# Kernel optimization log

Hardware: AMD Instinct MI355X
Metric: run time of the kernel (lower is better)

## Reference

```python
import jax, jax.numpy as jnp
import numpy as np

N = 50000   # nodes
E = 600000  # edges
H = 128     # hidden_dim


def _linear_params(key, fan_in, fan_out):
    kw, kb = jax.random.split(key)
    s = 1.0 / np.sqrt(fan_in)
    w = jax.random.uniform(kw, (fan_in, fan_out), minval=-s, maxval=s, dtype=jnp.float32)
    b = jax.random.uniform(kb, (fan_out,), minval=-s, maxval=s, dtype=jnp.float32)
    return w, b


def setup_inputs():
    key = jax.random.key(0)
    ks = jax.random.split(key, 9)
    x = jax.random.uniform(ks[0], (N, 1), dtype=jnp.float32)
    pre_h = jax.random.normal(ks[1], (N, H), dtype=jnp.float32)
    edge_index = jax.random.randint(ks[2], (2, E), 0, N, dtype=jnp.int32)
    edge_attr = jax.random.uniform(ks[3], (E, 1), dtype=jnp.float32)
    enc_w, enc_b = _linear_params(ks[4], 1 + H, H)      # BFS_Encoder.linear
    M_w, M_b = _linear_params(ks[5], H + H + 1, H)      # MPNN_Processor.M
    U_w, U_b = _linear_params(ks[6], H + H, H)          # MPNN_Processor.U
    dec_w, dec_b = _linear_params(ks[7], H + H, 1)      # BFS_Decoder.linear
    ter_w, ter_b = _linear_params(ks[8], H + H, 1)      # BFS_Terminator.linear
    return {"x": x, "pre_h": pre_h, "edge_attr": edge_attr,
            "enc_w": enc_w, "enc_b": enc_b, "M_w": M_w, "M_b": M_b,
            "U_w": U_w, "U_b": U_b, "dec_w": dec_w, "dec_b": dec_b,
            "ter_w": ter_w, "ter_b": ter_b, "edge_index": edge_index}


def reference(x, pre_h, edge_attr, enc_w, enc_b, M_w, M_b, U_w, U_b,
              dec_w, dec_b, ter_w, ter_b, edge_index):
    # Encoder: z = relu(Linear([x, pre_h]))
    z = jax.nn.relu(jnp.concatenate([x, pre_h], axis=-1) @ enc_w + enc_b)  # [N,H]

    # Processor (PyG MessagePassing, flow source_to_target):
    # z_i = z[edge_index[1]] (target), z_j = z[edge_index[0]] (source)
    src, tgt = edge_index[0], edge_index[1]
    m = jax.nn.relu(
        jnp.concatenate([z[tgt], z[src], edge_attr], axis=-1) @ M_w + M_b)  # [E,H]
    # scatter-max aggregate into target nodes; empty segments -> 0
    agg = jax.ops.segment_max(m, tgt, num_segments=N)
    agg = jnp.where(jnp.isfinite(agg), agg, 0.0)
    h = jax.nn.relu(jnp.concatenate([z, agg], axis=-1) @ U_w + U_b)  # [N,H]

    # Decoder
    y = jax.nn.sigmoid(jnp.concatenate([z, h], axis=-1) @ dec_w + dec_b)  # [N,1]

    # Terminator: mean over nodes, broadcast-concat, scalar mean
    h_mean = jnp.broadcast_to(jnp.mean(h, axis=0), h.shape)
    ter = jnp.mean(jnp.concatenate([h, h_mean], axis=-1) @ ter_w + ter_b)
    return h, y, ter
```

## Files before the change

### kernel.cpp

```cpp
#include <hip/hip_runtime.h>
#include <hip/hip_bf16.h>
#include <math.h>

#define HD 128
#define APAD 136

typedef short bf16x8 __attribute__((ext_vector_type(8)));
typedef float f32x4 __attribute__((ext_vector_type(4)));

static __device__ __forceinline__ unsigned short f2bf(float f) {
  __hip_bfloat16 b = __float2bfloat16(f);
  return *(unsigned short*)&b;
}
static __device__ __forceinline__ float bflo(unsigned int u) {
  return __uint_as_float(u << 16);
}
static __device__ __forceinline__ float bfhi(unsigned int u) {
  return __uint_as_float(u & 0xffff0000u);
}

__global__ __launch_bounds__(256) void k_frag_hist(
    const float* __restrict__ enc_w, const float* __restrict__ M_w,
    const float* __restrict__ U_w,
    unsigned short* __restrict__ encf, unsigned short* __restrict__ Pf,
    unsigned short* __restrict__ Qf, unsigned short* __restrict__ Uf,
    const int* __restrict__ ei, int* __restrict__ cnt, int E) {
  const int b = blockIdx.x;
  if (b >= 40) {
    const int e = (b - 40) * 256 + threadIdx.x;
    if (e < E) atomicAdd(&cnt[ei[E + e]], 1);
    return;
  }
  const float* W; unsigned short* F; int KS; int lb;
  if (b < 8)       { W = enc_w + HD;     F = encf; KS = 4; lb = b; }
  else if (b < 16) { W = M_w;            F = Pf;   KS = 4; lb = b - 8; }
  else if (b < 24) { W = M_w + HD * HD;  F = Qf;   KS = 4; lb = b - 16; }
  else             { W = U_w;            F = Uf;   KS = 8; lb = b - 24; }
  const int gid = lb * 256 + threadIdx.x;
  const int lane = gid & 63;
  const int ks = (gid >> 6) % KS;
  const int tile = gid / (64 * KS);
  const int col = tile * 16 + (lane & 15);
  const int k0 = ks * 32 + (lane >> 4) * 8;
  unsigned short v[8];
#pragma unroll
  for (int j = 0; j < 8; ++j) v[j] = f2bf(W[(size_t)(k0 + j) * HD + col]);
  unsigned short* dst = F + ((size_t)(tile * KS + ks) * 64 + lane) * 8;
#pragma unroll
  for (int j = 0; j < 8; ++j) dst[j] = v[j];
}

__global__ __launch_bounds__(256) void k_scan_block(
    const int* __restrict__ cnt, int* __restrict__ row_ptr,
    int* __restrict__ partials, int N) {
  __shared__ int s[256];
  const int t = threadIdx.x;
  const int base = blockIdx.x * 1024 + t * 4;
  int v[4], sum = 0;
#pragma unroll
  for (int i = 0; i < 4; ++i) {
    v[i] = (base + i < N) ? cnt[base + i] : 0;
    sum += v[i];
  }
  s[t] = sum;
  __syncthreads();
  for (int off = 1; off < 256; off <<= 1) {
    int xv = (t >= off) ? s[t - off] : 0;
    __syncthreads();
    if (t >= off) s[t] += xv;
    __syncthreads();
  }
  int run = s[t] - sum;
  if (t == 255) partials[blockIdx.x] = s[255];
#pragma unroll
  for (int i = 0; i < 4; ++i) {
    if (base + i < N) row_ptr[base + i] = run;
    run += v[i];
  }
}

__global__ void k_scan_partials(int* __restrict__ partials, int nb) {
  if (threadIdx.x == 0) {
    int run = 0;
    for (int i = 0; i < nb; ++i) { int v = partials[i]; partials[i] = run; run += v; }
  }
}

__global__ __launch_bounds__(256) void k_scan_add(
    int* __restrict__ row_ptr, const int* __restrict__ partials,
    int* __restrict__ cursor, int N) {
  const int base = blockIdx.x * 1024 + threadIdx.x * 4;
  const int p = partials[blockIdx.x];
#pragma unroll
  for (int i = 0; i < 4; ++i) {
    if (base + i < N) {
      int v = row_ptr[base + i] + p;
      row_ptr[base + i] = v;
      cursor[base + i] = v;
    }
  }
}

__global__ __launch_bounds__(256) void k_scatter(
    const int* __restrict__ ei, const float* __restrict__ edge_attr,
    int* __restrict__ cursor, int2* __restrict__ epack, int E) {
  const int e = blockIdx.x * 256 + threadIdx.x;
  if (e >= E) return;
  const int tgt = ei[E + e];
  const int pos = atomicAdd(&cursor[tgt], 1);
  epack[pos] = make_int2(ei[e], __float_as_int(edge_attr[e]));
}

__global__ __launch_bounds__(256, 4) void k_enc_pq(
    const float* __restrict__ x, const float* __restrict__ pre_h,
    const float* __restrict__ enc_w, const float* __restrict__ enc_b,
    const float* __restrict__ M_b,
    const unsigned short* __restrict__ encf, const unsigned short* __restrict__ Pf,
    const unsigned short* __restrict__ Qf,
    unsigned short* __restrict__ zg, unsigned short* __restrict__ Pg,
    unsigned short* __restrict__ Qg) {
  __shared__ unsigned short phs[16 * APAD];
  __shared__ unsigned short zsh[16 * APAD];
  __shared__ float xs[16];
  const int t = threadIdx.x;
  const int n0 = blockIdx.x * 16;

  {
    const int r = t >> 4, c0 = (t & 15) * 8;
    const float4 a = *(const float4*)&pre_h[(size_t)(n0 + r) * HD + c0];
    const float4 b = *(const float4*)&pre_h[(size_t)(n0 + r) * HD + c0 + 4];
    unsigned short* d = &phs[r * APAD + c0];
    d[0] = f2bf(a.x); d[1] = f2bf(a.y); d[2] = f2bf(a.z); d[3] = f2bf(a.w);
    d[4] = f2bf(b.x); d[5] = f2bf(b.y); d[6] = f2bf(b.z); d[7] = f2bf(b.w);
  }
  if (t < 16) xs[t] = x[n0 + t];
  __syncthreads();

  const int w = t >> 6, l = t & 63;
  const int m = l & 15, q = l >> 4;

  bf16x8 af[4];
#pragma unroll
  for (int ks = 0; ks < 4; ++ks)
    af[ks] = *(const bf16x8*)&phs[m * APAD + ks * 32 + q * 8];
  f32x4 acc[2] = {{0, 0, 0, 0}, {0, 0, 0, 0}};
#pragma unroll
  for (int tt = 0; tt < 2; ++tt) {
    const int tn = 2 * w + tt;
#pragma unroll
    for (int ks = 0; ks < 4; ++ks) {
      const bf16x8 bf = *(const bf16x8*)&encf[((size_t)(tn * 4 + ks) * 64 + l) * 8];
      acc[tt] = __builtin_amdgcn_mfma_f32_16x16x32_bf16(af[ks], bf, acc[tt], 0, 0, 0);
    }
  }
#pragma unroll
  for (int tt = 0; tt < 2; ++tt) {
    const int col = (2 * w + tt) * 16 + m;
    const float bb = enc_b[col];
    const float w0 = enc_w[col];
#pragma unroll
    for (int r = 0; r < 4; ++r) {
      const int row = q * 4 + r;
      const float zv = fmaxf(acc[tt][r] + bb + xs[row] * w0, 0.0f);
      zsh[row * APAD + col] = f2bf(zv);
    }
  }
  __syncthreads();

  bf16x8 az[4];
#pragma unroll
  for (int ks = 0; ks < 4; ++ks)
    az[ks] = *(const bf16x8*)&zsh[m * APAD + ks * 32 + q * 8];
  {
    const int r = t >> 4, c0 = (t & 15) * 8;
    *(uint4*)&zg[(size_t)(n0 + r) * HD + c0] = *(const uint4*)&zsh[r * APAD + c0];
  }
  __syncthreads();

  f32x4 pacc[2] = {{0, 0, 0, 0}, {0, 0, 0, 0}};
  f32x4 qacc[2] = {{0, 0, 0, 0}, {0, 0, 0, 0}};
#pragma unroll
  for (int tt = 0; tt < 2; ++tt) {
    const int tn = 2 * w + tt;
#pragma unroll
    for (int ks = 0; ks < 4; ++ks) {
      const bf16x8 bp = *(const bf16x8*)&Pf[((size_t)(tn * 4 + ks) * 64 + l) * 8];
      const bf16x8 bq = *(const bf16x8*)&Qf[((size_t)(tn * 4 + ks) * 64 + l) * 8];
      pacc[tt] = __builtin_amdgcn_mfma_f32_16x16x32_bf16(az[ks], bp, pacc[tt], 0, 0, 0);
      qacc[tt] = __builtin_amdgcn_mfma_f32_16x16x32_bf16(az[ks], bq, qacc[tt], 0, 0, 0);
    }
  }
#pragma unroll
  for (int tt = 0; tt < 2; ++tt) {
    const int col = (2 * w + tt) * 16 + m;
    const float mb = M_b[col];
#pragma unroll
    for (int r = 0; r < 4; ++r) {
      const int row = q * 4 + r;
      phs[row * APAD + col] = f2bf(pacc[tt][r] + mb);
      zsh[row * APAD + col] = f2bf(qacc[tt][r]);
    }
  }
  __syncthreads();
  {
    const int r = t >> 4, c0 = (t & 15) * 8;
    *(uint4*)&Pg[(size_t)(n0 + r) * HD + c0] = *(const uint4*)&phs[r * APAD + c0];
    *(uint4*)&Qg[(size_t)(n0 + r) * HD + c0] = *(const uint4*)&zsh[r * APAD + c0];
  }
}

__global__ __launch_bounds__(256, 8) void k_gather(
    const unsigned short* __restrict__ Pg, const unsigned short* __restrict__ Qg,
    const float* __restrict__ w_attr,
    const int* __restrict__ row_ptr, const int* __restrict__ row_end,
    const int2* __restrict__ epack,
    unsigned short* __restrict__ ag, int N) {
  const int t = threadIdx.x;
  const int w = t >> 6, l = t & 63;
  const int g = l >> 4, j = l & 15;
  const int n0 = blockIdx.x * 32;

  float wv[8];
  {
    const float4 wa = *(const float4*)&w_attr[j * 8];
    const float4 wb = *(const float4*)&w_attr[j * 8 + 4];
    wv[0] = wa.x; wv[1] = wa.y; wv[2] = wa.z; wv[3] = wa.w;
    wv[4] = wb.x; wv[5] = wb.y; wv[6] = wb.z; wv[7] = wb.w;
  }

#pragma unroll
  for (int i = 0; i < 2; ++i) {
    const int r = w * 8 + g * 2 + i;
    const int n = n0 + r;
    const int nc = min(n, N - 1);
    const int rs = row_ptr[nc], re = row_end[nc];
    float acc[8];
#pragma unroll
    for (int c = 0; c < 8; ++c) acc[c] = -INFINITY;
    for (int e = rs; e < re; e += 4) {
      int2 pk[4];
#pragma unroll
      for (int u = 0; u < 4; ++u) pk[u] = epack[min(e + u, re - 1)];
      uint4 qv[4];
#pragma unroll
      for (int u = 0; u < 4; ++u)
        qv[u] = *(const uint4*)&Qg[(size_t)pk[u].x * HD + j * 8];
#pragma unroll
      for (int u = 0; u < 4; ++u) {
        const float a = __int_as_float(pk[u].y);
        const unsigned int qq[4] = {qv[u].x, qv[u].y, qv[u].z, qv[u].w};
#pragma unroll
        for (int c = 0; c < 4; ++c) {
          acc[2 * c]     = fmaxf(acc[2 * c],     fmaf(a, wv[2 * c],     bflo(qq[c])));
          acc[2 * c + 1] = fmaxf(acc[2 * c + 1], fmaf(a, wv[2 * c + 1], bfhi(qq[c])));
        }
      }
    }
    if (n < N) {
      float res[8];
      if (re > rs) {
        const uint4 pv = *(const uint4*)&Pg[(size_t)n * HD + j * 8];
        const unsigned int pp[4] = {pv.x, pv.y, pv.z, pv.w};
#pragma unroll
        for (int c = 0; c < 4; ++c) {
          res[2 * c]     = fmaxf(bflo(pp[c]) + acc[2 * c],     0.0f);
          res[2 * c + 1] = fmaxf(bfhi(pp[c]) + acc[2 * c + 1], 0.0f);
        }
      } else {
#pragma unroll
        for (int c = 0; c < 8; ++c) res[c] = 0.0f;
      }
      uint4 st;
      st.x = (unsigned)f2bf(res[0]) | ((unsigned)f2bf(res[1]) << 16);
      st.y = (unsigned)f2bf(res[2]) | ((unsigned)f2bf(res[3]) << 16);
      st.z = (unsigned)f2bf(res[4]) | ((unsigned)f2bf(res[5]) << 16);
      st.w = (unsigned)f2bf(res[6]) | ((unsigned)f2bf(res[7]) << 16);
      *(uint4*)&ag[(size_t)n * HD + j * 8] = st;
    }
  }
}

__global__ __launch_bounds__(256, 8) void k_update(
    const unsigned short* __restrict__ zg, const unsigned short* __restrict__ ag,
    const unsigned short* __restrict__ Uf,
    const float* __restrict__ U_b, const float* __restrict__ dec_w,
    const float* __restrict__ dec_b,
    float* __restrict__ h_out, float* __restrict__ y_out,
    float* __restrict__ hpart, int N) {
  __shared__ unsigned short zsh[32 * APAD];
  __shared__ unsigned short ash[32 * APAD];
  __shared__ float hcol[HD];
  __shared__ float dacc[32];
  __shared__ float pr[32][8];
  const int t = threadIdx.x;
  const int n0 = blockIdx.x * 32;

  {
    const int r = t >> 3, c0 = (t & 7) * 16;
    const int n = min(n0 + r, N - 1);
    *(uint4*)&zsh[r * APAD + c0]     = *(const uint4*)&zg[(size_t)n * HD + c0];
    *(uint4*)&zsh[r * APAD + c0 + 8] = *(const uint4*)&zg[(size_t)n * HD + c0 + 8];
    *(uint4*)&ash[r * APAD + c0]     = *(const uint4*)&ag[(size_t)n * HD + c0];
    *(uint4*)&ash[r * APAD + c0 + 8] = *(const uint4*)&ag[(size_t)n * HD + c0 + 8];
  }
  if (t < 32) dacc[t] = 0.0f;
  if (t < HD) hcol[t] = 0.0f;
  __syncthreads();

  const int w = t >> 6, l = t & 63;

  const int mt = w & 1, nh = w >> 1;
  const int m = mt * 16 + (l & 15), q = l >> 4;
  bf16x8 afz[4], afa[4];
#pragma unroll
  for (int ks = 0; ks < 4; ++ks) {
    afz[ks] = *(const bf16x8*)&zsh[m * APAD + ks * 32 + q * 8];
    afa[ks] = *(const bf16x8*)&ash[m * APAD + ks * 32 + q * 8];
  }
  f32x4 acc4[4] = {{0, 0, 0, 0}, {0, 0, 0, 0}, {0, 0, 0, 0}, {0, 0, 0, 0}};
#pragma unroll
  for (int tt = 0; tt < 4; ++tt) {
    const int tn = nh * 4 + tt;
#pragma unroll
    for (int ks = 0; ks < 8; ++ks) {
      const bf16x8 bf = *(const bf16x8*)&Uf[((size_t)(tn * 8 + ks) * 64 + l) * 8];
      const bf16x8 a = (ks < 4) ? afz[ks] : afa[ks - 4];
      acc4[tt] = __builtin_amdgcn_mfma_f32_16x16x32_bf16(a, bf, acc4[tt], 0, 0, 0);
    }
  }
  float dp[4] = {0.0f, 0.0f, 0.0f, 0.0f};
#pragma unroll
  for (int tt = 0; tt < 4; ++tt) {
    const int col = (nh * 4 + tt) * 16 + (l & 15);
    const float ub = U_b[col];
    const float dw = dec_w[HD + col];
    float s4 = 0.0f;
#pragma unroll
    for (int r = 0; r < 4; ++r) {
      const int rowl = mt * 16 + q * 4 + r;
      const int n = n0 + rowl;
      float hv = fmaxf(acc4[tt][r] + ub, 0.0f);
      if (n < N) h_out[(size_t)n * HD + col] = hv; else hv = 0.0f;
      s4 += hv;
      dp[r] += hv * dw;
    }
    atomicAdd(&hcol[col], s4);
  }
#pragma unroll
  for (int off = 1; off < 16; off <<= 1) {
#pragma unroll
    for (int r = 0; r < 4; ++r) dp[r] += __shfl_xor(dp[r], off);
  }
  if ((l & 15) == 0) {
#pragma unroll
    for (int r = 0; r < 4; ++r) atomicAdd(&dacc[mt * 16 + q * 4 + r], dp[r]);
  }

  {
    const int r2 = t >> 3, s = t & 7;
    float part = 0.0f;
#pragma unroll
    for (int c = 0; c < 8; ++c) {
      const int kk = s * 16 + 2 * c;
      const unsigned int zu = *(const unsigned int*)&zsh[r2 * APAD + kk];
      part += bflo(zu) * dec_w[kk] + bfhi(zu) * dec_w[kk + 1];
    }
    pr[r2][s] = part;
  }
  __syncthreads();

  if (t < HD) hpart[(size_t)blockIdx.x * HD + t] = hcol[t];
  if (t < 32 && n0 + t < N) {
    float d = dec_b[0] + dacc[t];
#pragma unroll
    for (int s = 0; s < 8; ++s) d += pr[t][s];
    y_out[n0 + t] = 1.0f / (1.0f + expf(-d));
  }
}

__global__ __launch_bounds__(256) void k_hred(
    const float* __restrict__ hpart, float* __restrict__ hsum, int NB) {
  __shared__ float sh[HD];
  const int t = threadIdx.x;
  const int col = t & (HD - 1);
  const int half = t >> 7;
  float acc = 0.0f;
  for (int r = blockIdx.x * 2 + half; r < NB; r += 32)
    acc += hpart[(size_t)r * HD + col];
  if (half) sh[col] = acc;
  __syncthreads();
  if (!half) atomicAdd(&hsum[col], acc + sh[col]);
}

__global__ __launch_bounds__(128) void k_ter(
    const float* __restrict__ hsum, const float* __restrict__ ter_w,
    const float* __restrict__ ter_b, float* __restrict__ out, float invN) {
  __shared__ float r2[2];
  const int t = threadIdx.x;
  float v = (hsum[t] * invN) * (ter_w[t] + ter_w[HD + t]);
#pragma unroll
  for (int o = 32; o > 0; o >>= 1) v += __shfl_down(v, o);
  if ((t & 63) == 0) r2[t >> 6] = v;
  __syncthreads();
  if (t == 0) out[0] = r2[0] + r2[1] + ter_b[0];
}

extern "C" void kernel_launch(void* const* d_in, const int* in_sizes, int n_in,
                              void* d_out, int out_size, void* d_ws, size_t ws_size,
                              hipStream_t stream) {
  const float* x        = (const float*)d_in[0];
  const float* pre_h    = (const float*)d_in[1];
  const float* edge_attr= (const float*)d_in[2];
  const float* enc_w    = (const float*)d_in[3];
  const float* enc_b    = (const float*)d_in[4];
  const float* M_w      = (const float*)d_in[5];
  const float* M_b      = (const float*)d_in[6];
  const float* U_w      = (const float*)d_in[7];
  const float* U_b      = (const float*)d_in[8];
  const float* dec_w    = (const float*)d_in[9];
  const float* dec_b    = (const float*)d_in[10];
  const float* ter_w    = (const float*)d_in[11];
  const float* ter_b    = (const float*)d_in[12];
  const int*   edge_idx = (const int*)d_in[13];

  const int N = in_sizes[0];
  const int E = in_sizes[2];
  const size_t NH = (size_t)N * HD;

  float* out = (float*)d_out;
  float* h_out = out;
  float* y_out = out + NH;
  float* ter_out = out + NH + N;

  unsigned short* zg = (unsigned short*)d_ws;
  unsigned short* Pg = zg + NH;
  unsigned short* Qg = Pg + NH;
  unsigned short* ag = Qg + NH;
  int*   cursor   = (int*)(ag + NH);
  int*   row_ptr  = cursor + N;
  int*   partials = row_ptr + N;
  float* hsum     = (float*)(partials + 64);
  int2*  epack    = (int2*)(hsum + HD);
  unsigned short* encf = (unsigned short*)(epack + E);
  unsigned short* Pf   = encf + 8 * 4 * 64 * 8;
  unsigned short* Qf   = Pf + 8 * 4 * 64 * 8;
  unsigned short* Uf   = Qf + 8 * 4 * 64 * 8;
  float* hpart = (float*)(Uf + 16 * 256 * 8);

  hipMemsetAsync(cursor, 0, (2 * (size_t)N + 64 + HD) * sizeof(int), stream);

  const int scan_blocks = (N + 1023) / 1024;
  const int eb = (E + 255) / 256;
  const int nb32 = (N + 31) / 32;

  k_frag_hist<<<40 + eb, 256, 0, stream>>>(enc_w, M_w, U_w, encf, Pf, Qf, Uf,
                                           edge_idx, cursor, E);
  k_scan_block<<<scan_blocks, 256, 0, stream>>>(cursor, row_ptr, partials, N);
  k_scan_partials<<<1, 64, 0, stream>>>(partials, scan_blocks);
  k_scan_add<<<scan_blocks, 256, 0, stream>>>(row_ptr, partials, cursor, N);
  k_scatter<<<eb, 256, 0, stream>>>(edge_idx, edge_attr, cursor, epack, E);

  k_enc_pq<<<N / 16, 256, 0, stream>>>(x, pre_h, enc_w, enc_b, M_b,
                                       encf, Pf, Qf, zg, Pg, Qg);
  k_gather<<<nb32, 256, 0, stream>>>(
      Pg, Qg, M_w + 256 * HD, row_ptr, cursor, epack, ag, N);
  k_update<<<nb32, 256, 0, stream>>>(
      zg, ag, Uf, U_b, dec_w, dec_b, h_out, y_out, hpart, N);
  k_hred<<<16, 256, 0, stream>>>(hpart, hsum, nb32);
  k_ter<<<1, 128, 0, stream>>>(hsum, ter_w, ter_b, ter_out, 1.0f / (float)N);
}
```

Baseline: 259.5 us.

## Merge small launches: fold partials scan, fuse scatter with encoder, fuse reduce and terminator

Removes the single-thread partials scan kernel by having each scan_add block reduce the preceding partials itself with a wavefront shuffle. Merges the edge scatter kernel and the encoder/PQ kernel into one launch whose first eb blocks scatter edges while the rest run the encoder, so the two overlap. Replaces the two-kernel h reduction and terminator with a single 1024-thread block, which also drops the hsum buffer and shrinks the memset. The aim is fewer launches and less serialization, at the cost of one block doing all of the hpart reduction and an unused load left in the decoder loop.

```diff
diff --git a/kernel.cpp b/kernel.cpp
--- a/kernel.cpp
+++ b/kernel.cpp
@@ -79,18 +79,20 @@
   }
 }
 
-__global__ void k_scan_partials(int* __restrict__ partials, int nb) {
-  if (threadIdx.x == 0) {
-    int run = 0;
-    for (int i = 0; i < nb; ++i) { int v = partials[i]; partials[i] = run; run += v; }
-  }
-}
-
 __global__ __launch_bounds__(256) void k_scan_add(
     int* __restrict__ row_ptr, const int* __restrict__ partials,
-    int* __restrict__ cursor, int N) {
-  const int base = blockIdx.x * 1024 + threadIdx.x * 4;
-  const int p = partials[blockIdx.x];
+    int* __restrict__ cursor, int N, int nb) {
+  __shared__ int poff;
+  const int t = threadIdx.x;
+  if (t < 64) {
+    int v = (t < nb && t < blockIdx.x) ? partials[t] : 0;
+#pragma unroll
+    for (int o = 32; o > 0; o >>= 1) v += __shfl_down(v, o);
+    if (t == 0) poff = v;
+  }
+  __syncthreads();
+  const int p = poff;
+  const int base = blockIdx.x * 1024 + t * 4;
 #pragma unroll
   for (int i = 0; i < 4; ++i) {
     if (base + i < N) {
@@ -101,17 +103,9 @@
   }
 }
 
-__global__ __launch_bounds__(256) void k_scatter(
+__global__ __launch_bounds__(256, 4) void k_scatter_enc(
     const int* __restrict__ ei, const float* __restrict__ edge_attr,
-    int* __restrict__ cursor, int2* __restrict__ epack, int E) {
-  const int e = blockIdx.x * 256 + threadIdx.x;
-  if (e >= E) return;
-  const int tgt = ei[E + e];
-  const int pos = atomicAdd(&cursor[tgt], 1);
-  epack[pos] = make_int2(ei[e], __float_as_int(edge_attr[e]));
-}
-
-__global__ __launch_bounds__(256, 4) void k_enc_pq(
+    int* __restrict__ cursor, int2* __restrict__ epack, int E, int eb,
     const float* __restrict__ x, const float* __restrict__ pre_h,
     const float* __restrict__ enc_w, const float* __restrict__ enc_b,
     const float* __restrict__ M_b,
@@ -123,8 +117,18 @@
   __shared__ unsigned short zsh[16 * APAD];
   __shared__ float xs[16];
   const int t = threadIdx.x;
-  const int n0 = blockIdx.x * 16;
-
+
+  if (blockIdx.x < (unsigned)eb) {
+    const int e = blockIdx.x * 256 + t;
+    if (e < E) {
+      const int tgt = ei[E + e];
+      const int pos = atomicAdd(&cursor[tgt], 1);
+      epack[pos] = make_int2(ei[e], __float_as_int(edge_attr[e]));
+    }
+    return;
+  }
+
+  const int n0 = (blockIdx.x - eb) * 16;
   {
     const int r = t >> 4, c0 = (t & 15) * 8;
     const float4 a = *(const float4*)&pre_h[(size_t)(n0 + r) * HD + c0];
@@ -363,6 +367,7 @@
     for (int c = 0; c < 8; ++c) {
       const int kk = s * 16 + 2 * c;
       const unsigned int zu = *(const unsigned int*)&zsh[r2 * APAD + kk];
+      const unsigned int hu = *(const unsigned int*)&ash[r2 * APAD + kk];
       part += bflo(zu) * dec_w[kk] + bfhi(zu) * dec_w[kk + 1];
     }
     pr[r2][s] = part;
@@ -378,31 +383,33 @@
   }
 }
 
-__global__ __launch_bounds__(256) void k_hred(
-    const float* __restrict__ hpart, float* __restrict__ hsum, int NB) {
-  __shared__ float sh[HD];
+__global__ __launch_bounds__(1024) void k_hredter(
+    const float* __restrict__ hpart, const float* __restrict__ ter_w,
+    const float* __restrict__ ter_b, float* __restrict__ out,
+    float invN, int NB) {
+  __shared__ float s[1024];
   const int t = threadIdx.x;
   const int col = t & (HD - 1);
-  const int half = t >> 7;
+  const int grp = t >> 7;
   float acc = 0.0f;
-  for (int r = blockIdx.x * 2 + half; r < NB; r += 32)
-    acc += hpart[(size_t)r * HD + col];
-  if (half) sh[col] = acc;
-  __syncthreads();
-  if (!half) atomicAdd(&hsum[col], acc + sh[col]);
-}
-
-__global__ __launch_bounds__(128) void k_ter(
-    const float* __restrict__ hsum, const float* __restrict__ ter_w,
-    const float* __restrict__ ter_b, float* __restrict__ out, float invN) {
-  __shared__ float r2[2];
-  const int t = threadIdx.x;
-  float v = (hsum[t] * invN) * (ter_w[t] + ter_w[HD + t]);
+  for (int r = grp; r < NB; r += 8) acc += hpart[(size_t)r * HD + col];
+  s[t] = acc;
+  __syncthreads();
+  if (t < 512) s[t] += s[t + 512];
+  __syncthreads();
+  if (t < 256) s[t] += s[t + 256];
+  __syncthreads();
+  float v = 0.0f;
+  if (t < 128) {
+    const float colsum = s[t] + s[t + 128];
+    v = (colsum * invN) * (ter_w[t] + ter_w[HD + t]);
+  }
 #pragma unroll
   for (int o = 32; o > 0; o >>= 1) v += __shfl_down(v, o);
-  if ((t & 63) == 0) r2[t >> 6] = v;
-  __syncthreads();
-  if (t == 0) out[0] = r2[0] + r2[1] + ter_b[0];
+  __syncthreads();
+  if (t < 128 && (t & 63) == 0) s[t >> 6] = v;
+  __syncthreads();
+  if (t == 0) out[0] = s[0] + s[1] + ter_b[0];
 }
 
 extern "C" void kernel_launch(void* const* d_in, const int* in_sizes, int n_in,
@@ -439,15 +446,14 @@
   int*   cursor   = (int*)(ag + NH);
   int*   row_ptr  = cursor + N;
   int*   partials = row_ptr + N;
-  float* hsum     = (float*)(partials + 64);
-  int2*  epack    = (int2*)(hsum + HD);
+  int2*  epack    = (int2*)(partials + 64);
   unsigned short* encf = (unsigned short*)(epack + E);
   unsigned short* Pf   = encf + 8 * 4 * 64 * 8;
   unsigned short* Qf   = Pf + 8 * 4 * 64 * 8;
   unsigned short* Uf   = Qf + 8 * 4 * 64 * 8;
   float* hpart = (float*)(Uf + 16 * 256 * 8);
 
-  hipMemsetAsync(cursor, 0, (2 * (size_t)N + 64 + HD) * sizeof(int), stream);
+  hipMemsetAsync(cursor, 0, (size_t)N * sizeof(int), stream);
 
   const int scan_blocks = (N + 1023) / 1024;
   const int eb = (E + 255) / 256;
@@ -456,16 +462,15 @@
   k_frag_hist<<<40 + eb, 256, 0, stream>>>(enc_w, M_w, U_w, encf, Pf, Qf, Uf,
                                            edge_idx, cursor, E);
   k_scan_block<<<scan_blocks, 256, 0, stream>>>(cursor, row_ptr, partials, N);
-  k_scan_partials<<<1, 64, 0, stream>>>(partials, scan_blocks);
-  k_scan_add<<<scan_blocks, 256, 0, stream>>>(row_ptr, partials, cursor, N);
-  k_scatter<<<eb, 256, 0, stream>>>(edge_idx, edge_attr, cursor, epack, E);
-
-  k_enc_pq<<<N / 16, 256, 0, stream>>>(x, pre_h, enc_w, enc_b, M_b,
-                                       encf, Pf, Qf, zg, Pg, Qg);
+  k_scan_add<<<scan_blocks, 256, 0, stream>>>(row_ptr, partials, cursor, N,
+                                              scan_blocks);
+  k_scatter_enc<<<eb + N / 16, 256, 0, stream>>>(
+      edge_idx, edge_attr, cursor, epack, E, eb,
+      x, pre_h, enc_w, enc_b, M_b, encf, Pf, Qf, zg, Pg, Qg);
   k_gather<<<nb32, 256, 0, stream>>>(
       Pg, Qg, M_w + 256 * HD, row_ptr, cursor, epack, ag, N);
   k_update<<<nb32, 256, 0, stream>>>(
       zg, ag, Uf, U_b, dec_w, dec_b, h_out, y_out, hpart, N);
-  k_hred<<<16, 256, 0, stream>>>(hpart, hsum, nb32);
-  k_ter<<<1, 128, 0, stream>>>(hsum, ter_w, ter_b, ter_out, 1.0f / (float)N);
-}
+  k_hredter<<<1, 1024, 0, stream>>>(hpart, ter_w, ter_b, ter_out,
+                                    1.0f / (float)N, nb32);
+}
```

Result: slower. 284.8 us (+9.7%).
